# Performance work log

Measured on AMD Instinct MI355X. Metric: run time of the kernel, lower is better.

## Reference

```python
import jax, jax.numpy as jnp
import numpy as np

N_WIRES = 16
DIM = 2 ** N_WIRES
BSZ = 512
FFN_DIM = 64
N_BLOCKS = 2
N_RAND_OPS = 20
EPS = 1e-5


def rx_mat(theta):
    c = jnp.cos(theta / 2).astype(jnp.complex64)
    s = jnp.sin(theta / 2).astype(jnp.complex64)
    i = jnp.complex64(1j)
    return jnp.stack([jnp.stack([c, -i * s]), jnp.stack([-i * s, c])])


def ry_mat(theta):
    c = jnp.cos(theta / 2).astype(jnp.complex64)
    s = jnp.sin(theta / 2).astype(jnp.complex64)
    return jnp.stack([jnp.stack([c, -s]), jnp.stack([s, c])])


def apply_1q(psi, U, wire):
    # psi: [bsz, 2**n]; apply 2x2 U on `wire` (wire 0 = most significant)
    b = psi.shape[0]
    left = 2 ** wire
    s = psi.reshape(b, left, 2, -1)
    out = jnp.einsum('ij,bljr->blir', U, s)
    return out.reshape(b, -1)


def apply_cnot(psi, cw, tw):
    b = psi.shape[0]
    x = psi.reshape((b,) + (2,) * N_WIRES)
    x = jnp.moveaxis(x, (1 + cw, 1 + tw), (1, 2))
    x = jnp.concatenate([x[:, :1], x[:, 1:2, ::-1]], axis=1)
    x = jnp.moveaxis(x, (1, 2), (1 + cw, 1 + tw))
    return x.reshape(b, -1)


def measure_z(psi):
    # <Z_w> for every wire -> [bsz, n]
    b = psi.shape[0]
    p = jnp.abs(psi) ** 2
    outs = []
    for w in range(N_WIRES):
        pr = p.reshape(b, 2 ** w, 2, -1)
        outs.append((pr[:, :, 0] - pr[:, :, 1]).sum(axis=(1, 2)))
    return jnp.stack(outs, axis=1)


def layernorm(x, g, b):
    mu = x.mean(-1, keepdims=True)
    var = ((x - mu) ** 2).mean(-1, keepdims=True)
    return (x - mu) * jax.lax.rsqrt(var + EPS) * g + b


def setup_inputs() -> dict:
    key = jax.random.key(0)
    ks = jax.random.split(key, 16)
    states = jax.random.normal(ks[0], (BSZ, DIM), dtype=jnp.float32)
    rand_angles = jax.random.uniform(ks[1], (N_RAND_OPS,), minval=0.0, maxval=2 * np.pi, dtype=jnp.float32)
    theta_rx = jax.random.normal(ks[2], (N_BLOCKS,), dtype=jnp.float32)
    theta_ry = jax.random.normal(ks[3], (N_BLOCKS,), dtype=jnp.float32)
    s1 = 1.0 / np.sqrt(N_WIRES)
    s2 = 1.0 / np.sqrt(FFN_DIM)
    w1 = jax.random.uniform(ks[4], (N_BLOCKS, FFN_DIM, N_WIRES), minval=-s1, maxval=s1, dtype=jnp.float32)
    b1 = jax.random.uniform(ks[5], (N_BLOCKS, FFN_DIM), minval=-s1, maxval=s1, dtype=jnp.float32)
    w2 = jax.random.uniform(ks[6], (N_BLOCKS, N_WIRES, FFN_DIM), minval=-s2, maxval=s2, dtype=jnp.float32)
    b2 = jax.random.uniform(ks[7], (N_BLOCKS, N_WIRES), minval=-s2, maxval=s2, dtype=jnp.float32)
    g1 = jnp.ones((N_BLOCKS, N_WIRES), jnp.float32)
    be1 = jnp.zeros((N_BLOCKS, N_WIRES), jnp.float32)
    g2 = jnp.ones((N_BLOCKS, N_WIRES), jnp.float32)
    be2 = jnp.zeros((N_BLOCKS, N_WIRES), jnp.float32)
    wh = jax.random.uniform(ks[8], (1, N_WIRES), minval=-s1, maxval=s1, dtype=jnp.float32)
    bh = jax.random.uniform(ks[9], (1,), minval=-s1, maxval=s1, dtype=jnp.float32)
    return dict(states=states, rand_angles=rand_angles, theta_rx=theta_rx, theta_ry=theta_ry,
                w1=w1, b1=b1, w2=w2, b2=b2, g1=g1, be1=be1, g2=g2, be2=be2, wh=wh, bh=bh)


def _forward(states, rand_angles, theta_rx, theta_ry, w1, b1, w2, b2, g1, be1, g2, be2, wh, bh):
    # amplitude encoding: normalize, cast to complex statevector
    psi = (states / jnp.linalg.norm(states, axis=1, keepdims=True)).astype(jnp.complex64)
    # deterministic stand-in for tq.RandomLayer(n_ops=20): cycle RX/RY/CNOT over wires
    for i in range(N_RAND_OPS):
        w = (i * 5) % N_WIRES
        k = i % 3
        if k == 0:
            psi = apply_1q(psi, rx_mat(rand_angles[i]), w)
        elif k == 1:
            psi = apply_1q(psi, ry_mat(rand_angles[i]), w)
        else:
            psi = apply_cnot(psi, w, (w + 1) % N_WIRES)
    feats = None
    for blk in range(N_BLOCKS):
        # attention sub-module: shared RX on every wire, CNOT ring, measure Z
        Urx = rx_mat(theta_rx[blk])
        for w in range(N_WIRES):
            psi = apply_1q(psi, Urx, w)
        for w in range(N_WIRES - 1):
            psi = apply_cnot(psi, w, w + 1)
        psi = apply_cnot(psi, N_WIRES - 1, 0)
        attn = measure_z(psi)
        x = layernorm(attn, g1[blk], be1[blk])
        # ffn sub-module: shared RY on every wire, measure, MLP (dropout=eval identity)
        Ury = ry_mat(theta_ry[blk])
        for w in range(N_WIRES):
            psi = apply_1q(psi, Ury, w)
        m = measure_z(psi)
        h = jax.nn.relu(m @ w1[blk].T + b1[blk])
        ffn = h @ w2[blk].T + b2[blk]
        feats = layernorm(x + ffn, g2[blk], be2[blk])
    return (feats @ wh.T + bh)[:, 0]


def reference(states, rand_angles, theta_rx, theta_ry, w1, b1, w2, b2, g1, be1, g2, be2, wh, bh):
    return _forward(states, rand_angles, theta_rx, theta_ry, w1, b1, w2, b2, g1, be1, g2, be2, wh, bh)
```

## Files before the change

kernel.cpp:

```cpp
#include <hip/hip_runtime.h>
#include <math.h>


#define NT 256
#define ACCS 40
#define BSZQ 512

typedef float v2f __attribute__((ext_vector_type(2)));
typedef __fp16 h2t __attribute__((ext_vector_type(2)));

__device__ __forceinline__ v2f mk2(float a, float b){ v2f r; r.x = a; r.y = b; return r; }

__device__ __forceinline__ void wave_fence(){
  asm volatile("" ::: "memory");
  __builtin_amdgcn_wave_barrier();
  asm volatile("" ::: "memory");
}

__device__ __forceinline__ unsigned int f2h(v2f a){
  h2t h = __builtin_amdgcn_cvt_pkrtz(a.x, a.y);
  return *(unsigned int*)&h;
}
__device__ __forceinline__ v2f h2f(unsigned int u){
  h2t h = *(h2t*)&u;
  return mk2((float)h.x, (float)h.y);
}

__device__ __forceinline__ v2f pk_mul(v2f a, v2f b){
  v2f d; asm("v_pk_mul_f32 %0, %1, %2" : "=v"(d) : "v"(a), "v"(b)); return d;
}
__device__ __forceinline__ void pk_fma_acc(v2f& c, v2f a, v2f b){
  asm("v_pk_fma_f32 %0, %1, %2, %0" : "+v"(c) : "v"(a), "v"(b));
}
__device__ __forceinline__ void pk_fma_sw_acc(v2f& c, v2f a, v2f b){
  asm("v_pk_fma_f32 %0, %1, %2, %0 op_sel:[1,0,0] op_sel_hi:[0,1,1]"
      : "+v"(c) : "v"(a), "v"(b));
}
__device__ __forceinline__ void pk_add_acc(v2f& c, v2f a){
  asm("v_pk_add_f32 %0, %1, %0" : "+v"(c) : "v"(a));
}

struct C2 { float r, i; };
struct G1Q { C2 a, b, c, d; };

__device__ __forceinline__ C2 cmul(C2 x, C2 y){ return C2{ x.r*y.r - x.i*y.i, x.r*y.i + x.i*y.r }; }
__device__ __forceinline__ C2 cadd(C2 x, C2 y){ return C2{ x.r + y.r, x.i + y.i }; }
__device__ __forceinline__ G1Q mkRX(float th){
  float cc = cosf(0.5f*th), ss = sinf(0.5f*th);
  return G1Q{ C2{cc,0.f}, C2{0.f,-ss}, C2{0.f,-ss}, C2{cc,0.f} };
}
__device__ __forceinline__ G1Q mkRY(float th){
  float cc = cosf(0.5f*th), ss = sinf(0.5f*th);
  return G1Q{ C2{cc,0.f}, C2{-ss,0.f}, C2{ss,0.f}, C2{cc,0.f} };
}
__device__ __forceinline__ G1Q gmul(G1Q A, G1Q B){
  return G1Q{ cadd(cmul(A.a,B.a), cmul(A.b,B.c)),
              cadd(cmul(A.a,B.b), cmul(A.b,B.d)),
              cadd(cmul(A.c,B.a), cmul(A.d,B.c)),
              cadd(cmul(A.c,B.b), cmul(A.d,B.d)) };
}

struct PG1Q { v2f aR, aI, bR, bI, cR, cI, dR, dI; };
__device__ __forceinline__ PG1Q loadPG(const float* __restrict__ gt, int i){
  const float4* p = (const float4*)(gt + i*8);
  float4 u = p[0], w = p[1];
  PG1Q g;
  g.aR = mk2(u.x, u.x); g.aI = mk2(-u.y, u.y);
  g.bR = mk2(u.z, u.z); g.bI = mk2(-u.w, u.w);
  g.cR = mk2(w.x, w.x); g.cI = mk2(-w.y, w.y);
  g.dR = mk2(w.z, w.z); g.dI = mk2(-w.w, w.w);
  return g;
}

__device__ __forceinline__ int SW(int i){ return (i & ~15) | ((i ^ (i>>4) ^ (i>>8)) & 15); }

template<int M>
__device__ __forceinline__ float swzx(float x){
  return __int_as_float(__builtin_amdgcn_ds_swizzle(__float_as_int(x), (M<<10)|0x1F));
}
template<int C>
__device__ __forceinline__ float dppx(float x){
  return __int_as_float(__builtin_amdgcn_mov_dpp(__float_as_int(x), C, 0xF, 0xF, true));
}
template<int N>
__device__ __forceinline__ void wsumB(float* x){
  #pragma unroll
  for (int i=0;i<N;i++) x[i] += dppx<0xB1>(x[i]);
  #pragma unroll
  for (int i=0;i<N;i++) x[i] += dppx<0x4E>(x[i]);
  #pragma unroll
  for (int i=0;i<N;i++) x[i] += swzx<4>(x[i]);
  #pragma unroll
  for (int i=0;i<N;i++) x[i] += swzx<8>(x[i]);
  #pragma unroll
  for (int i=0;i<N;i++) x[i] += swzx<16>(x[i]);
  #pragma unroll
  for (int i=0;i<N;i++)
    x[i] = __int_as_float(__builtin_amdgcn_readlane(__float_as_int(x[i]), 0)) +
           __int_as_float(__builtin_amdgcn_readlane(__float_as_int(x[i]), 32));
}

__device__ __forceinline__ void greg16p(v2f* v, const PG1Q g, const int q){
  const int bq = 1<<q;
  #pragma unroll
  for (int r=0;r<16;r++){
    if (r & bq) continue;
    v2f a0 = v[r], a1 = v[r|bq];
    v2f t0 = pk_mul(a0, g.aR);
    pk_fma_sw_acc(t0, a0, g.aI);
    pk_fma_acc   (t0, a1, g.bR);
    pk_fma_sw_acc(t0, a1, g.bI);
    v2f t1 = pk_mul(a0, g.cR);
    pk_fma_sw_acc(t1, a0, g.cI);
    pk_fma_acc   (t1, a1, g.dR);
    pk_fma_sw_acc(t1, a1, g.dI);
    v[r] = t0; v[r|bq] = t1;
  }
}
__device__ __forceinline__ void creg16(v2f* v, const int qc, const int qt){
  #pragma unroll
  for (int r=0;r<16;r++){
    if ((r & (1<<qc)) && !(r & (1<<qt))){
      v2f tmp = v[r]; v[r] = v[r|(1<<qt)]; v[r|(1<<qt)] = tmp;
    }
  }
}
__device__ __forceinline__ float xdot16p(const v2f* v, const int m){
  v2f s = pk_mul(v[0], v[m]);
  #pragma unroll
  for (int r=1;r<16;r++) pk_fma_acc(s, v[r], v[r^m]);
  return s.x + s.y;
}

__global__ void qs_prep(const float* __restrict__ ra, const float* __restrict__ trx,
                        const float* __restrict__ tryv, float* __restrict__ gt){
  if (threadIdx.x != 0) return;
  float trx0 = trx[0];
  G1Q RX0 = mkRX(trx0);
  G1Q g[14];
  g[0]  = gmul(RX0, gmul(mkRY(ra[19]), mkRX(ra[3])));
  g[1]  = mkRX(trx0 + ra[6]);
  g[2]  = mkRX(trx0 + ra[9]);
  g[3]  = mkRX(trx0 + ra[12]);
  g[4]  = mkRX(trx0 + ra[15]);
  g[5]  = mkRX(trx0 + ra[18]);
  g[6]  = RX0;
  g[7]  = gmul(RX0, mkRY(ra[4]));
  g[8]  = mkRY(ra[1]);
  g[9]  = gmul(RX0, mkRY(ra[7]));
  g[10] = gmul(RX0, mkRY(ra[10]));
  g[11] = gmul(RX0, mkRY(ra[13]));
  g[12] = gmul(RX0, gmul(mkRY(ra[16]), mkRX(ra[0])));
  g[13] = gmul(mkRX(trx[1]), mkRY(tryv[0]));
  for (int i=0;i<14;i++){
    gt[i*8+0]=g[i].a.r; gt[i*8+1]=g[i].a.i;
    gt[i*8+2]=g[i].b.r; gt[i*8+3]=g[i].b.i;
    gt[i*8+4]=g[i].c.r; gt[i*8+5]=g[i].c.i;
    gt[i*8+6]=g[i].d.r; gt[i*8+7]=g[i].d.i;
  }
}

__global__ __launch_bounds__(NT) void qs_p1(const float* __restrict__ x, const float* __restrict__ gt,
                                            unsigned int* __restrict__ psi, float* __restrict__ acc){
  __shared__ __align__(16) v2f s[2048];
  int b = blockIdx.x >> 4, t = blockIdx.x & 15;
  int tid = threadIdx.x;
  if (t == 0 && tid < ACCS) acc[b*ACCS + tid] = 0.f;
  v2f v[16];
  const float4* xb = (const float4*)(x + (size_t)b*65536 + t*4096 + tid*16);
  #pragma unroll
  for (int q=0;q<4;q++){
    float4 f = xb[q];
    v[4*q+0] = mk2(f.x, 0.f);
    v[4*q+1] = mk2(f.y, 0.f);
    v[4*q+2] = mk2(f.z, 0.f);
    v[4*q+3] = mk2(f.w, 0.f);
  }
  greg16p(v, loadPG(gt,0), 0);
  greg16p(v, loadPG(gt,1), 1);
  greg16p(v, loadPG(gt,2), 2);
  greg16p(v, loadPG(gt,3), 3);
  {
    int wbase = ((tid&15)<<3) | ((tid>>4)<<7);
    int rbase = (tid&7) | ((tid>>4)<<7);
    v2f tmp[8];
    #pragma unroll
    for (int j=0;j<8;j++) s[SW(j | wbase)] = v[j];
    wave_fence();
    if (!(tid & 8)){
      #pragma unroll
      for (int r=0;r<8;r++)  v[r]     = s[SW(rbase | (r<<3))];
      #pragma unroll
      for (int r=8;r<16;r++) tmp[r-8] = s[SW(rbase | (r<<3))];
    }
    wave_fence();
    #pragma unroll
    for (int j=8;j<16;j++) s[SW((j&7) | wbase)] = v[j];
    wave_fence();
    if (tid & 8){
      #pragma unroll
      for (int r=0;r<16;r++) v[r] = s[SW(rbase | (r<<3))];
    } else {
      #pragma unroll
      for (int r=8;r<16;r++) v[r] = tmp[r-8];
    }
  }
  creg16(v, 1, 0);
  creg16(v, 2, 1);
  creg16(v, 3, 2);
  {
    bool c8 = (tid & 16);
    #pragma unroll
    for (int r=0;r<8;r++){
      v2f lo = v[r], hi = v[r|8];
      v[r]   = c8 ? hi : lo;
      v[r|8] = c8 ? lo : hi;
    }
  }
  greg16p(v, loadPG(gt,4), 0);
  greg16p(v, loadPG(gt,5), 1);
  PG1Q PG6 = loadPG(gt,6);
  greg16p(v, PG6, 2);
  greg16p(v, PG6, 3);
  unsigned int* pbL = psi + (size_t)b*65536 + t*4096;
  #pragma unroll
  for (int r=0;r<16;r++) pbL[(tid&15) | (r<<4) | ((tid>>4)<<8)] = f2h(v[r]);
}

__global__ __launch_bounds__(NT) void qs_p2(unsigned int* __restrict__ psi, const float* __restrict__ gt){
  __shared__ __align__(16) v2f s[2048];
  int b = blockIdx.x >> 4, t = blockIdx.x & 15;
  int tid = threadIdx.x;
  v2f v[16];
  unsigned int* pb = psi + (size_t)b*65536;
  #pragma unroll
  for (int r=0;r<16;r++)
    v[r] = h2f(pb[(tid&15) | (t<<4) | (r<<8) | ((tid>>4)<<12)]);
  greg16p(v, loadPG(gt,7), 3);
  greg16p(v, loadPG(gt,8), 2);
  creg16(v, 1, 0);
  creg16(v, 2, 1);
  PG1Q PG6 = loadPG(gt,6);
  greg16p(v, PG6, 2);
  greg16p(v, PG6, 1);
  greg16p(v, PG6, 0);
  {
    int wbase = ((tid>>4)&7) | ((tid&15)<<7);
    int rbase = ((tid>>4)<<3) | ((tid&15)<<7);
    v2f tmp[8];
    if (tid < 128){
      #pragma unroll
      for (int rr=0;rr<16;rr++) s[SW(wbase | (rr<<3))] = v[rr];
    }
    __syncthreads();
    #pragma unroll
    for (int r=0;r<8;r++) tmp[r] = s[SW(rbase | (r&7))];
    __syncthreads();
    if (tid >= 128){
      #pragma unroll
      for (int rr=0;rr<16;rr++) s[SW(wbase | (rr<<3))] = v[rr];
    }
    __syncthreads();
    #pragma unroll
    for (int r=8;r<16;r++) v[r] = s[SW(rbase | (r&7))];
    #pragma unroll
    for (int r=0;r<8;r++) v[r] = tmp[r];
  }
  greg16p(v, loadPG(gt,9), 0);
  greg16p(v, loadPG(gt,10), 1);
  greg16p(v, loadPG(gt,11), 2);
  greg16p(v, loadPG(gt,12), 3);
  #pragma unroll
  for (int r=0;r<16;r++)
    pb[(tid&15) | (t<<4) | ((tid>>4)<<8) | (r<<12)] = f2h(v[r]);
}

__global__ __launch_bounds__(NT) void qs_p4(unsigned int* __restrict__ psi, const float* __restrict__ gt,
                                            float* __restrict__ acc){
  __shared__ __align__(16) v2f s[2048];
  int b = blockIdx.x >> 4, t = blockIdx.x & 15;
  int tid = threadIdx.x;
  PG1Q U = loadPG(gt, 13);
  unsigned int* pb = psi + (size_t)b*65536;
  v2f v[16];
  {
    int Y = (tid>>4) | ((tid&15)<<4);
    int XH = Y ^ (Y>>1);
    int x7 = ((t>>3) ^ Y) & 1;
    int runbase = (XH<<8) | (x7<<7) | (((t ^ (t>>1)) & 7) << 4);
    const uint4* rp = (const uint4*)(pb + runbase);
    v2f tmp[16];
    #pragma unroll
    for (int q=0;q<4;q++){
      uint4 u = rp[q];
      tmp[4*q+0] = h2f(u.x);
      tmp[4*q+1] = h2f(u.y);
      tmp[4*q+2] = h2f(u.z);
      tmp[4*q+3] = h2f(u.w);
    }
    if (t & 1){
      v[15]=tmp[0];  v[14]=tmp[1];  v[12]=tmp[2];  v[13]=tmp[3];
      v[ 8]=tmp[4];  v[ 9]=tmp[5];  v[11]=tmp[6];  v[10]=tmp[7];
      v[ 0]=tmp[8];  v[ 1]=tmp[9];  v[ 3]=tmp[10]; v[ 2]=tmp[11];
      v[ 7]=tmp[12]; v[ 6]=tmp[13]; v[ 4]=tmp[14]; v[ 5]=tmp[15];
    } else {
      v[ 0]=tmp[0];  v[ 1]=tmp[1];  v[ 3]=tmp[2];  v[ 2]=tmp[3];
      v[ 7]=tmp[4];  v[ 6]=tmp[5];  v[ 4]=tmp[6];  v[ 5]=tmp[7];
      v[15]=tmp[8];  v[14]=tmp[9];  v[12]=tmp[10]; v[13]=tmp[11];
      v[ 8]=tmp[12]; v[ 9]=tmp[13]; v[11]=tmp[14]; v[10]=tmp[15];
    }
    #pragma unroll
    for (int r=1;r<16;r+=2){
      v[r].x = swzx<8>(v[r].x);
      v[r].y = swzx<8>(v[r].y);
    }
    greg16p(v, U, 0); greg16p(v, U, 1); greg16p(v, U, 2); greg16p(v, U, 3);
  }
  {
    int wbase = (tid&7) | ((tid>>4)<<7);
    int rbase = ((tid&15)<<3) | ((tid>>4)<<7);
    v2f tmp[8];
    if (!(tid & 8)){
      #pragma unroll
      for (int j=0;j<16;j++) s[SW(wbase | (j<<3))] = v[j];
    }
    wave_fence();
    #pragma unroll
    for (int r=0;r<8;r++) tmp[r] = s[SW((r&7) | rbase)];
    wave_fence();
    if (tid & 8){
      #pragma unroll
      for (int j=0;j<16;j++) s[SW(wbase | (j<<3))] = v[j];
    }
    wave_fence();
    #pragma unroll
    for (int r=8;r<16;r++) v[r] = s[SW((r&7) | rbase)];
    #pragma unroll
    for (int r=0;r<8;r++) v[r] = tmp[r];
  }
  float Xa, Xb, Xc, Xd;
  {
    greg16p(v, U, 0); greg16p(v, U, 1); greg16p(v, U, 2); greg16p(v, U, 3);
    creg16(v, 3, 2);
    creg16(v, 2, 1);
    creg16(v, 1, 0);
    Xa = xdot16p(v, 8);
    Xb = xdot16p(v, 4);
    Xc = xdot16p(v, 2);
    v2f XdP = mk2(0.f, 0.f);
    #pragma unroll
    for (int r=0;r<16;r++)
      pk_fma_acc(XdP, v[r], mk2(dppx<0xB1>(v[r^8].x), dppx<0xB1>(v[r^8].y)));
    Xd = XdP.x + XdP.y;
  }
  {
    int wbase = ((tid>>4)&7) | ((tid&15)<<7);
    int rbase = ((tid>>4)<<3) | ((tid&15)<<7);
    v2f tmp[8];
    __syncthreads();
    if (tid < 128){
      #pragma unroll
      for (int rr=0;rr<16;rr++) s[SW(wbase | (rr<<3))] = v[rr];
    }
    __syncthreads();
    #pragma unroll
    for (int r=0;r<8;r++) tmp[r] = s[SW(rbase | (r&7))];
    __syncthreads();
    if (tid >= 128){
      #pragma unroll
      for (int rr=0;rr<16;rr++) s[SW(wbase | (rr<<3))] = v[rr];
    }
    __syncthreads();
    #pragma unroll
    for (int r=8;r<16;r++) v[r] = s[SW(rbase | (r&7))];
    #pragma unroll
    for (int r=0;r<8;r++) v[r] = tmp[r];
  }
  float Xe, Xf, Xg, Xh;
  {
    greg16p(v, U, 0); greg16p(v, U, 1); greg16p(v, U, 2); greg16p(v, U, 3);
    {
      bool c12 = (tid & 16);
      #pragma unroll
      for (int r=0;r<8;r++){
        v2f lo = v[r], hi = v[r|8];
        v[r]   = c12 ? hi : lo;
        v[r|8] = c12 ? lo : hi;
      }
    }
    creg16(v, 3, 2);
    creg16(v, 2, 1);
    creg16(v, 1, 0);
    v2f XeP = mk2(0.f, 0.f);
    #pragma unroll
    for (int r=0;r<16;r++)
      pk_fma_acc(XeP, v[r], mk2(swzx<16>(v[r].x), swzx<16>(v[r].y)));
    Xe = XeP.x + XeP.y;
    Xf = xdot16p(v, 8);
    Xg = xdot16p(v, 4);
    Xh = xdot16p(v, 2);
    int Bs = (tid&15) | (t<<4) | ((tid>>4)<<12);
    int Cs = Bs ^ (Bs>>1);
    #pragma unroll
    for (int r=0;r<16;r++)
      pb[Cs ^ ((r<<8) ^ (r<<7))] = f2h(v[r]);
  }
  float vals[8] = {Xa, Xb, Xc, Xe, Xf, Xg, Xh, Xd};
  wsumB<8>(vals);
  if ((tid & 63) == 0){
    float* A = acc + b*ACCS;
    #pragma unroll
    for (int i=0;i<7;i++) atomicAdd(A+25+i, vals[i]);
    atomicAdd(A+32, vals[7]);
  }
}

__global__ __launch_bounds__(NT) void qs_p5(const unsigned int* __restrict__ psi, const float* __restrict__ gt,
                                            float* __restrict__ acc){
  int b = blockIdx.x >> 4, t = blockIdx.x & 15;
  int tid = threadIdx.x;
  PG1Q U = loadPG(gt, 13);
  const unsigned int* pb = psi + (size_t)b*65536;
  v2f v[16];
  int Bv = (t<<12) | ((tid>>4)<<8) | (tid&15);
  int Cg = Bv ^ (Bv>>1);
  #pragma unroll
  for (int r=0;r<16;r++)
    v[r] = h2f(pb[Cg ^ ((r<<4) ^ (r<<3))]);
  greg16p(v, U, 0); greg16p(v, U, 1); greg16p(v, U, 2); greg16p(v, U, 3);
  v2f z2 = mk2(0.f, 0.f);
  v2f totP=z2, S4P=z2, S5P=z2, S6P=z2, S7P=z2;
  #pragma unroll
  for (int r=0;r<16;r++){
    v2f sq = pk_mul(v[r], v[r]);
    pk_add_acc(totP, sq);
    if (__popc(r)&1)    pk_add_acc(S4P, sq);
    if (__popc(r>>1)&1) pk_add_acc(S5P, sq);
    if (__popc(r>>2)&1) pk_add_acc(S6P, sq);
    if (__popc(r>>3)&1) pk_add_acc(S7P, sq);
  }
  float totA = totP.x + totP.y;
  float S4l = S4P.x + S4P.y, S5l = S5P.x + S5P.y;
  float S6l = S6P.x + S6P.y, S7l = S7P.x + S7P.y;
  float S4h = totA - S4l;
  float S0 = (__popc(tid & 0x1F)&1) ? S4h : S4l;
  float S1 = (__popc(tid & 0x1E)&1) ? S4h : S4l;
  float S2 = (__popc(tid & 0x1C)&1) ? S4h : S4l;
  float S3 = (__popc(tid & 0x18)&1) ? S4h : S4l;
  bool u8 = (tid & 16);
  float S4 = u8 ? S4h : S4l;
  float S5 = u8 ? totA - S5l : S5l;
  float S6 = u8 ? totA - S6l : S6l;
  float S7 = u8 ? totA - S7l : S7l;
  float S8 = u8 ? totA : 0.f;
  float K9  = (tid & 32) ? totA : 0.f;
  float K10 = (tid & 64) ? totA : 0.f;
  float K11 = (tid & 128)? totA : 0.f;
  float X45 = xdot16p(v,3), X56 = xdot16p(v,6), X67 = xdot16p(v,12);
  v2f X01P=z2, X12P=z2, X23P=z2, X34P=z2, X78P=z2;
  #pragma unroll
  for (int r=0;r<16;r++){
    float vx = v[r].x, vy = v[r].y;
    pk_fma_acc(X01P, v[r], mk2(dppx<0x1B>(vx), dppx<0x1B>(vy)));
    pk_fma_acc(X12P, v[r], mk2(swzx<6>(vx),  swzx<6>(vy)));
    pk_fma_acc(X23P, v[r], mk2(swzx<12>(vx), swzx<12>(vy)));
    pk_fma_acc(X34P, v[r], mk2(swzx<8>(v[r^1].x), swzx<8>(v[r^1].y)));
    pk_fma_acc(X78P, v[r], mk2(swzx<16>(v[r^8].x), swzx<16>(v[r^8].y)));
  }
  float X01 = X01P.x + X01P.y, X12 = X12P.x + X12P.y, X23 = X23P.x + X23P.y;
  float X34 = X34P.x + X34P.y, X78 = X78P.x + X78P.y;
  float vals[21] = {totA, S0,S1,S2,S3,S4,S5,S6,S7,S8, K9,K10,K11,
                    X01,X12,X23,X34,X45,X56,X67,X78};
  wsumB<21>(vals);
  if ((tid & 63) == 0){
    float* A = acc + b*ACCS;
    atomicAdd(A+0, vals[0]);
    #pragma unroll
    for (int p=0;p<12;p++) atomicAdd(A+1+p, vals[1+p]);
    if (t&1) atomicAdd(A+13, vals[0]);
    if (t&2) atomicAdd(A+14, vals[0]);
    if (t&4) atomicAdd(A+15, vals[0]);
    float zz = vals[0] - 2.f*vals[1];
    if (t&8) zz = -zz;
    atomicAdd(A+16, zz);
    #pragma unroll
    for (int j=0;j<8;j++) atomicAdd(A+17+j, vals[13+j]);
  }
}

__global__ __launch_bounds__(256) void qs_tail(const float* __restrict__ acc, const float* __restrict__ tryv,
    const float* __restrict__ w1, const float* __restrict__ b1,
    const float* __restrict__ w2, const float* __restrict__ b2,
    const float* __restrict__ g1, const float* __restrict__ be1,
    const float* __restrict__ g2, const float* __restrict__ be2,
    const float* __restrict__ wh, const float* __restrict__ bh,
    float* __restrict__ out){
  int b = blockIdx.x * 256 + threadIdx.x;
  if (b >= BSZQ) return;
  const float* A = acc + b*ACCS;
  float tot = A[0];
  float inv = 1.f / tot;
  float Z[16], X[16];
  Z[0] = A[16] * inv;
  Z[1] = 1.f - 2.f*A[15]*inv;
  Z[2] = 1.f - 2.f*A[14]*inv;
  Z[3] = 1.f - 2.f*A[13]*inv;
  #pragma unroll
  for (int w=4; w<15; w++) Z[w] = 1.f - 2.f*A[1 + (15-w)]*inv;
  Z[15] = 1.f - 2.f*A[1]*inv;
  #pragma unroll
  for (int w=0; w<7; w++) X[w] = A[25+w]*inv;
  #pragma unroll
  for (int w=7; w<15; w++) X[w] = A[16 + (15-w)]*inv;
  X[15] = A[32]*inv;
  float th = tryv[1];
  float ct = cosf(th), st = sinf(th);
  float M4[16];
  #pragma unroll
  for (int w=0; w<16; w++) M4[w] = ct*Z[w] - st*X[w];
  float mu = 0.f;
  #pragma unroll
  for (int w=0; w<16; w++) mu += Z[w];
  mu *= (1.f/16.f);
  float var = 0.f;
  #pragma unroll
  for (int w=0; w<16; w++){ float d = Z[w]-mu; var += d*d; }
  var *= (1.f/16.f);
  float rs = rsqrtf(var + 1e-5f);
  float xln[16];
  #pragma unroll
  for (int w=0; w<16; w++) xln[w] = (Z[w]-mu)*rs*g1[16+w] + be1[16+w];
  float h[64];
  for (int j=0;j<64;j++){
    float sacc = b1[64 + j];
    #pragma unroll
    for (int w=0; w<16; w++) sacc += M4[w] * w1[1024 + j*16 + w];
    h[j] = fmaxf(sacc, 0.f);
  }
  float y[16];
  for (int w=0; w<16; w++){
    float sacc = b2[16 + w];
    #pragma unroll
    for (int j=0;j<64;j++) sacc += h[j] * w2[1024 + w*64 + j];
    y[w] = xln[w] + sacc;
  }
  mu = 0.f;
  #pragma unroll
  for (int w=0; w<16; w++) mu += y[w];
  mu *= (1.f/16.f);
  var = 0.f;
  #pragma unroll
  for (int w=0; w<16; w++){ float d = y[w]-mu; var += d*d; }
  var *= (1.f/16.f);
  rs = rsqrtf(var + 1e-5f);
  float o = bh[0];
  #pragma unroll
  for (int w=0; w<16; w++) o += ((y[w]-mu)*rs*g2[16+w] + be2[16+w]) * wh[w];
  out[b] = o;
}

extern "C" void kernel_launch(void* const* d_in, const int* in_sizes, int n_in,
                              void* d_out, int out_size, void* d_ws, size_t ws_size,
                              hipStream_t stream) {
  const float* states = (const float*)d_in[0];
  const float* ra     = (const float*)d_in[1];
  const float* trx    = (const float*)d_in[2];
  const float* tryv   = (const float*)d_in[3];
  const float* w1     = (const float*)d_in[4];
  const float* b1     = (const float*)d_in[5];
  const float* w2     = (const float*)d_in[6];
  const float* b2     = (const float*)d_in[7];
  const float* g1     = (const float*)d_in[8];
  const float* be1    = (const float*)d_in[9];
  const float* g2     = (const float*)d_in[10];
  const float* be2    = (const float*)d_in[11];
  const float* wh     = (const float*)d_in[12];
  const float* bh     = (const float*)d_in[13];
  float* out = (float*)d_out;

  unsigned int* psi = (unsigned int*)d_ws;
  float* acc  = (float*)((char*)d_ws + (size_t)BSZQ*65536*sizeof(float2));
  float* gt = out;

  dim3 g(BSZQ*16);
  qs_prep<<<1, 64, 0, stream>>>(ra, trx, tryv, gt);
  qs_p1<<<g, NT, 0, stream>>>(states, gt, psi, acc);
  qs_p2<<<g, NT, 0, stream>>>(psi, gt);
  qs_p4<<<g, NT, 0, stream>>>(psi, gt, acc);
  qs_p5<<<g, NT, 0, stream>>>(psi, gt, acc);
  qs_tail<<<2, 256, 0, stream>>>(acc, tryv, w1, b1, w2, b2, g1, be1, g2, be2, wh, bh, out);
}
```

Baseline: 535.8 us.

## Run gate math in packed fp16 and simplify LDS transposes in p2/p4/p5

Kernels p2, p4 and p5 now keep the state vector as packed half2 registers and apply gates with v_pk_fma_f16 instead of converting to fp32 and using v_pk_fma_f32. Expectation values use v_dot2_f32_f16, and the shared-memory transposes move 32-bit half2 words in a single pass with a new swizzle, rather than two staged passes of 64-bit values. Precomputed fp16 gate coefficients are stored after the fp32 table. This halves ALU work and LDS traffic and removes barriers, at the cost of fp16 rounding accumulating across gate applications.

After: 517.5 us. 3.4% less time.

```diff
diff --git a/kernel.cpp b/kernel.cpp
--- a/kernel.cpp
+++ b/kernel.cpp
@@ -17,13 +17,9 @@
   asm volatile("" ::: "memory");
 }
 
-__device__ __forceinline__ unsigned int f2h(v2f a){
+__device__ __forceinline__ unsigned f2h(v2f a){
   h2t h = __builtin_amdgcn_cvt_pkrtz(a.x, a.y);
-  return *(unsigned int*)&h;
-}
-__device__ __forceinline__ v2f h2f(unsigned int u){
-  h2t h = *(h2t*)&u;
-  return mk2((float)h.x, (float)h.y);
+  return *(unsigned*)&h;
 }
 
 __device__ __forceinline__ v2f pk_mul(v2f a, v2f b){
@@ -36,8 +32,19 @@
   asm("v_pk_fma_f32 %0, %1, %2, %0 op_sel:[1,0,0] op_sel_hi:[0,1,1]"
       : "+v"(c) : "v"(a), "v"(b));
 }
-__device__ __forceinline__ void pk_add_acc(v2f& c, v2f a){
-  asm("v_pk_add_f32 %0, %1, %0" : "+v"(c) : "v"(a));
+
+__device__ __forceinline__ unsigned pk16_mul(unsigned a, unsigned b){
+  unsigned d; asm("v_pk_mul_f16 %0, %1, %2" : "=v"(d) : "v"(a), "v"(b)); return d;
+}
+__device__ __forceinline__ void pk16_fma_acc(unsigned& c, unsigned a, unsigned b){
+  asm("v_pk_fma_f16 %0, %1, %2, %0" : "+v"(c) : "v"(a), "v"(b));
+}
+__device__ __forceinline__ void pk16_fma_sw_acc(unsigned& c, unsigned a, unsigned b){
+  asm("v_pk_fma_f16 %0, %1, %2, %0 op_sel:[1,0,0] op_sel_hi:[0,1,1]"
+      : "+v"(c) : "v"(a), "v"(b));
+}
+__device__ __forceinline__ void dot2acc(float& s, unsigned a, unsigned b){
+  asm("v_dot2_f32_f16 %0, %1, %2, %0" : "+v"(s) : "v"(a), "v"(b));
 }
 
 struct C2 { float r, i; };
@@ -71,12 +78,33 @@
   g.dR = mk2(w.z, w.z); g.dI = mk2(-w.w, w.w);
   return g;
 }
+struct PGH { unsigned aR, aI, bR, bI, cR, cI, dR, dI; };
+__device__ __forceinline__ PGH loadPGH(const float* __restrict__ gt, int i){
+  const uint4* p = (const uint4*)((const unsigned*)gt + 112 + i*8);
+  uint4 u = p[0], w = p[1];
+  return PGH{u.x, u.y, u.z, u.w, w.x, w.y, w.z, w.w};
+}
+__device__ __forceinline__ unsigned pkh(float lo, float hi){
+  __fp16 l = (__fp16)lo, h = (__fp16)hi;
+  unsigned short lb, hb;
+  __builtin_memcpy(&lb, &l, 2); __builtin_memcpy(&hb, &h, 2);
+  return (unsigned)lb | ((unsigned)hb<<16);
+}
 
 __device__ __forceinline__ int SW(int i){ return (i & ~15) | ((i ^ (i>>4) ^ (i>>8)) & 15); }
+__device__ __forceinline__ int SWB(int i){ return i ^ ((i>>8)&15) ^ (((i>>8)&1)<<4); }
 
 template<int M>
 __device__ __forceinline__ float swzx(float x){
   return __int_as_float(__builtin_amdgcn_ds_swizzle(__float_as_int(x), (M<<10)|0x1F));
+}
+template<int M>
+__device__ __forceinline__ unsigned swzu(unsigned x){
+  return (unsigned)__builtin_amdgcn_ds_swizzle((int)x, (M<<10)|0x1F);
+}
+template<int C>
+__device__ __forceinline__ unsigned dppu(unsigned x){
+  return (unsigned)__builtin_amdgcn_mov_dpp((int)x, C, 0xF, 0xF, true);
 }
 template<int C>
 __device__ __forceinline__ float dppx(float x){
@@ -117,6 +145,23 @@
     v[r] = t0; v[r|bq] = t1;
   }
 }
+__device__ __forceinline__ void greg16h(unsigned* v, const PGH g, const int q){
+  const int bq = 1<<q;
+  #pragma unroll
+  for (int r=0;r<16;r++){
+    if (r & bq) continue;
+    unsigned a0 = v[r], a1 = v[r|bq];
+    unsigned t0 = pk16_mul(a0, g.aR);
+    pk16_fma_sw_acc(t0, a0, g.aI);
+    pk16_fma_acc   (t0, a1, g.bR);
+    pk16_fma_sw_acc(t0, a1, g.bI);
+    unsigned t1 = pk16_mul(a0, g.cR);
+    pk16_fma_sw_acc(t1, a0, g.cI);
+    pk16_fma_acc   (t1, a1, g.dR);
+    pk16_fma_sw_acc(t1, a1, g.dI);
+    v[r] = t0; v[r|bq] = t1;
+  }
+}
 __device__ __forceinline__ void creg16(v2f* v, const int qc, const int qt){
   #pragma unroll
   for (int r=0;r<16;r++){
@@ -125,11 +170,19 @@
     }
   }
 }
-__device__ __forceinline__ float xdot16p(const v2f* v, const int m){
-  v2f s = pk_mul(v[0], v[m]);
-  #pragma unroll
-  for (int r=1;r<16;r++) pk_fma_acc(s, v[r], v[r^m]);
-  return s.x + s.y;
+__device__ __forceinline__ void creg16u(unsigned* v, const int qc, const int qt){
+  #pragma unroll
+  for (int r=0;r<16;r++){
+    if ((r & (1<<qc)) && !(r & (1<<qt))){
+      unsigned tmp = v[r]; v[r] = v[r|(1<<qt)]; v[r|(1<<qt)] = tmp;
+    }
+  }
+}
+__device__ __forceinline__ float xdot16h(const unsigned* v, const int m){
+  float s = 0.f;
+  #pragma unroll
+  for (int r=0;r<16;r++) dot2acc(s, v[r], v[r^m]);
+  return s;
 }
 
 __global__ void qs_prep(const float* __restrict__ ra, const float* __restrict__ trx,
@@ -158,10 +211,21 @@
     gt[i*8+4]=g[i].c.r; gt[i*8+5]=g[i].c.i;
     gt[i*8+6]=g[i].d.r; gt[i*8+7]=g[i].d.i;
   }
+  unsigned* gh = (unsigned*)gt + 112;
+  for (int i=0;i<14;i++){
+    gh[i*8+0] = pkh( g[i].a.r,  g[i].a.r);
+    gh[i*8+1] = pkh(-g[i].a.i,  g[i].a.i);
+    gh[i*8+2] = pkh( g[i].b.r,  g[i].b.r);
+    gh[i*8+3] = pkh(-g[i].b.i,  g[i].b.i);
+    gh[i*8+4] = pkh( g[i].c.r,  g[i].c.r);
+    gh[i*8+5] = pkh(-g[i].c.i,  g[i].c.i);
+    gh[i*8+6] = pkh( g[i].d.r,  g[i].d.r);
+    gh[i*8+7] = pkh(-g[i].d.i,  g[i].d.i);
+  }
 }
 
 __global__ __launch_bounds__(NT) void qs_p1(const float* __restrict__ x, const float* __restrict__ gt,
-                                            unsigned int* __restrict__ psi, float* __restrict__ acc){
+                                            unsigned* __restrict__ psi, float* __restrict__ acc){
   __shared__ __align__(16) v2f s[2048];
   int b = blockIdx.x >> 4, t = blockIdx.x & 15;
   int tid = threadIdx.x;
@@ -222,81 +286,65 @@
   PG1Q PG6 = loadPG(gt,6);
   greg16p(v, PG6, 2);
   greg16p(v, PG6, 3);
-  unsigned int* pbL = psi + (size_t)b*65536 + t*4096;
+  unsigned* pbL = psi + (size_t)b*65536 + t*4096;
   #pragma unroll
   for (int r=0;r<16;r++) pbL[(tid&15) | (r<<4) | ((tid>>4)<<8)] = f2h(v[r]);
 }
 
-__global__ __launch_bounds__(NT) void qs_p2(unsigned int* __restrict__ psi, const float* __restrict__ gt){
-  __shared__ __align__(16) v2f s[2048];
+__global__ __launch_bounds__(NT) void qs_p2(unsigned* __restrict__ psi, const float* __restrict__ gt){
+  __shared__ unsigned s[4096];
   int b = blockIdx.x >> 4, t = blockIdx.x & 15;
   int tid = threadIdx.x;
-  v2f v[16];
-  unsigned int* pb = psi + (size_t)b*65536;
+  int a = tid & 15, g = tid >> 4;
+  unsigned v[16];
+  unsigned* pb = psi + (size_t)b*65536;
   #pragma unroll
   for (int r=0;r<16;r++)
-    v[r] = h2f(pb[(tid&15) | (t<<4) | (r<<8) | ((tid>>4)<<12)]);
-  greg16p(v, loadPG(gt,7), 3);
-  greg16p(v, loadPG(gt,8), 2);
-  creg16(v, 1, 0);
-  creg16(v, 2, 1);
-  PG1Q PG6 = loadPG(gt,6);
-  greg16p(v, PG6, 2);
-  greg16p(v, PG6, 1);
-  greg16p(v, PG6, 0);
-  {
-    int wbase = ((tid>>4)&7) | ((tid&15)<<7);
-    int rbase = ((tid>>4)<<3) | ((tid&15)<<7);
-    v2f tmp[8];
-    if (tid < 128){
-      #pragma unroll
-      for (int rr=0;rr<16;rr++) s[SW(wbase | (rr<<3))] = v[rr];
-    }
-    __syncthreads();
-    #pragma unroll
-    for (int r=0;r<8;r++) tmp[r] = s[SW(rbase | (r&7))];
-    __syncthreads();
-    if (tid >= 128){
-      #pragma unroll
-      for (int rr=0;rr<16;rr++) s[SW(wbase | (rr<<3))] = v[rr];
-    }
-    __syncthreads();
-    #pragma unroll
-    for (int r=8;r<16;r++) v[r] = s[SW(rbase | (r&7))];
-    #pragma unroll
-    for (int r=0;r<8;r++) v[r] = tmp[r];
-  }
-  greg16p(v, loadPG(gt,9), 0);
-  greg16p(v, loadPG(gt,10), 1);
-  greg16p(v, loadPG(gt,11), 2);
-  greg16p(v, loadPG(gt,12), 3);
+    v[r] = pb[a | (t<<4) | (r<<8) | (g<<12)];
+  greg16h(v, loadPGH(gt,7), 3);
+  greg16h(v, loadPGH(gt,8), 2);
+  creg16u(v, 1, 0);
+  creg16u(v, 2, 1);
+  PGH G6 = loadPGH(gt,6);
+  greg16h(v, G6, 2);
+  greg16h(v, G6, 1);
+  greg16h(v, G6, 0);
+  #pragma unroll
+  for (int r=0;r<16;r++) s[SWB(a | (g<<4) | (r<<8))] = v[r];
+  __syncthreads();
+  #pragma unroll
+  for (int r=0;r<16;r++) v[r] = s[SWB(a | (r<<4) | (g<<8))];
+  greg16h(v, loadPGH(gt,9), 0);
+  greg16h(v, loadPGH(gt,10), 1);
+  greg16h(v, loadPGH(gt,11), 2);
+  greg16h(v, loadPGH(gt,12), 3);
   #pragma unroll
   for (int r=0;r<16;r++)
-    pb[(tid&15) | (t<<4) | ((tid>>4)<<8) | (r<<12)] = f2h(v[r]);
-}
-
-__global__ __launch_bounds__(NT) void qs_p4(unsigned int* __restrict__ psi, const float* __restrict__ gt,
+    pb[a | (t<<4) | (g<<8) | (r<<12)] = v[r];
+}
+
+__global__ __launch_bounds__(NT) void qs_p4(unsigned* __restrict__ psi, const float* __restrict__ gt,
                                             float* __restrict__ acc){
-  __shared__ __align__(16) v2f s[2048];
+  __shared__ unsigned s[4096];
   int b = blockIdx.x >> 4, t = blockIdx.x & 15;
   int tid = threadIdx.x;
-  PG1Q U = loadPG(gt, 13);
-  unsigned int* pb = psi + (size_t)b*65536;
-  v2f v[16];
+  PGH U = loadPGH(gt, 13);
+  unsigned* pb = psi + (size_t)b*65536;
+  unsigned v[16];
   {
     int Y = (tid>>4) | ((tid&15)<<4);
     int XH = Y ^ (Y>>1);
     int x7 = ((t>>3) ^ Y) & 1;
     int runbase = (XH<<8) | (x7<<7) | (((t ^ (t>>1)) & 7) << 4);
     const uint4* rp = (const uint4*)(pb + runbase);
-    v2f tmp[16];
+    unsigned tmp[16];
     #pragma unroll
     for (int q=0;q<4;q++){
       uint4 u = rp[q];
-      tmp[4*q+0] = h2f(u.x);
-      tmp[4*q+1] = h2f(u.y);
-      tmp[4*q+2] = h2f(u.z);
-      tmp[4*q+3] = h2f(u.w);
+      tmp[4*q+0] = u.x;
+      tmp[4*q+1] = u.y;
+      tmp[4*q+2] = u.z;
+      tmp[4*q+3] = u.w;
     }
     if (t & 1){
       v[15]=tmp[0];  v[14]=tmp[1];  v[12]=tmp[2];  v[13]=tmp[3];
@@ -310,100 +358,63 @@
       v[ 8]=tmp[12]; v[ 9]=tmp[13]; v[11]=tmp[14]; v[10]=tmp[15];
     }
     #pragma unroll
-    for (int r=1;r<16;r+=2){
-      v[r].x = swzx<8>(v[r].x);
-      v[r].y = swzx<8>(v[r].y);
-    }
-    greg16p(v, U, 0); greg16p(v, U, 1); greg16p(v, U, 2); greg16p(v, U, 3);
-  }
-  {
-    int wbase = (tid&7) | ((tid>>4)<<7);
-    int rbase = ((tid&15)<<3) | ((tid>>4)<<7);
-    v2f tmp[8];
-    if (!(tid & 8)){
-      #pragma unroll
-      for (int j=0;j<16;j++) s[SW(wbase | (j<<3))] = v[j];
-    }
-    wave_fence();
-    #pragma unroll
-    for (int r=0;r<8;r++) tmp[r] = s[SW((r&7) | rbase)];
-    wave_fence();
-    if (tid & 8){
-      #pragma unroll
-      for (int j=0;j<16;j++) s[SW(wbase | (j<<3))] = v[j];
-    }
-    wave_fence();
-    #pragma unroll
-    for (int r=8;r<16;r++) v[r] = s[SW((r&7) | rbase)];
-    #pragma unroll
-    for (int r=0;r<8;r++) v[r] = tmp[r];
-  }
+    for (int r=1;r<16;r+=2) v[r] = swzu<8>(v[r]);
+    greg16h(v, U, 0); greg16h(v, U, 1); greg16h(v, U, 2); greg16h(v, U, 3);
+    #pragma unroll
+    for (int j=0;j<16;j++)
+      s[SWB(j | ((tid>>4)<<4) | ((tid&15)<<8))] = v[j];
+  }
+  wave_fence();
   float Xa, Xb, Xc, Xd;
   {
-    greg16p(v, U, 0); greg16p(v, U, 1); greg16p(v, U, 2); greg16p(v, U, 3);
-    creg16(v, 3, 2);
-    creg16(v, 2, 1);
-    creg16(v, 1, 0);
-    Xa = xdot16p(v, 8);
-    Xb = xdot16p(v, 4);
-    Xc = xdot16p(v, 2);
-    v2f XdP = mk2(0.f, 0.f);
     #pragma unroll
     for (int r=0;r<16;r++)
-      pk_fma_acc(XdP, v[r], mk2(dppx<0xB1>(v[r^8].x), dppx<0xB1>(v[r^8].y)));
-    Xd = XdP.x + XdP.y;
-  }
-  {
-    int wbase = ((tid>>4)&7) | ((tid&15)<<7);
-    int rbase = ((tid>>4)<<3) | ((tid&15)<<7);
-    v2f tmp[8];
-    __syncthreads();
-    if (tid < 128){
-      #pragma unroll
-      for (int rr=0;rr<16;rr++) s[SW(wbase | (rr<<3))] = v[rr];
-    }
-    __syncthreads();
-    #pragma unroll
-    for (int r=0;r<8;r++) tmp[r] = s[SW(rbase | (r&7))];
-    __syncthreads();
-    if (tid >= 128){
-      #pragma unroll
-      for (int rr=0;rr<16;rr++) s[SW(wbase | (rr<<3))] = v[rr];
-    }
-    __syncthreads();
-    #pragma unroll
-    for (int r=8;r<16;r++) v[r] = s[SW(rbase | (r&7))];
-    #pragma unroll
-    for (int r=0;r<8;r++) v[r] = tmp[r];
-  }
+      v[r] = s[SWB((tid&15) | ((tid>>4)<<4) | (r<<8))];
+    greg16h(v, U, 0); greg16h(v, U, 1); greg16h(v, U, 2); greg16h(v, U, 3);
+    creg16u(v, 3, 2);
+    creg16u(v, 2, 1);
+    creg16u(v, 1, 0);
+    Xa = xdot16h(v, 8);
+    Xb = xdot16h(v, 4);
+    Xc = xdot16h(v, 2);
+    Xd = 0.f;
+    #pragma unroll
+    for (int r=0;r<16;r++) dot2acc(Xd, v[r], dppu<0xB1>(v[r^8]));
+    wave_fence();
+    #pragma unroll
+    for (int r=0;r<16;r++)
+      s[SWB((tid&15) | ((tid>>4)<<4) | (r<<8))] = v[r];
+  }
+  __syncthreads();
   float Xe, Xf, Xg, Xh;
   {
-    greg16p(v, U, 0); greg16p(v, U, 1); greg16p(v, U, 2); greg16p(v, U, 3);
+    #pragma unroll
+    for (int r=0;r<16;r++)
+      v[r] = s[SWB((tid&15) | (r<<4) | ((tid>>4)<<8))];
+    greg16h(v, U, 0); greg16h(v, U, 1); greg16h(v, U, 2); greg16h(v, U, 3);
     {
       bool c12 = (tid & 16);
       #pragma unroll
       for (int r=0;r<8;r++){
-        v2f lo = v[r], hi = v[r|8];
+        unsigned lo = v[r], hi = v[r|8];
         v[r]   = c12 ? hi : lo;
         v[r|8] = c12 ? lo : hi;
       }
     }
-    creg16(v, 3, 2);
-    creg16(v, 2, 1);
-    creg16(v, 1, 0);
-    v2f XeP = mk2(0.f, 0.f);
-    #pragma unroll
-    for (int r=0;r<16;r++)
-      pk_fma_acc(XeP, v[r], mk2(swzx<16>(v[r].x), swzx<16>(v[r].y)));
-    Xe = XeP.x + XeP.y;
-    Xf = xdot16p(v, 8);
-    Xg = xdot16p(v, 4);
-    Xh = xdot16p(v, 2);
+    creg16u(v, 3, 2);
+    creg16u(v, 2, 1);
+    creg16u(v, 1, 0);
+    Xe = 0.f;
+    #pragma unroll
+    for (int r=0;r<16;r++) dot2acc(Xe, v[r], swzu<16>(v[r]));
+    Xf = xdot16h(v, 8);
+    Xg = xdot16h(v, 4);
+    Xh = xdot16h(v, 2);
     int Bs = (tid&15) | (t<<4) | ((tid>>4)<<12);
     int Cs = Bs ^ (Bs>>1);
     #pragma unroll
     for (int r=0;r<16;r++)
-      pb[Cs ^ ((r<<8) ^ (r<<7))] = f2h(v[r]);
+      pb[Cs ^ ((r<<8) ^ (r<<7))] = v[r];
   }
   float vals[8] = {Xa, Xb, Xc, Xe, Xf, Xg, Xh, Xd};
   wsumB<8>(vals);
@@ -415,33 +426,28 @@
   }
 }
 
-__global__ __launch_bounds__(NT) void qs_p5(const unsigned int* __restrict__ psi, const float* __restrict__ gt,
+__global__ __launch_bounds__(NT) void qs_p5(const unsigned* __restrict__ psi, const float* __restrict__ gt,
                                             float* __restrict__ acc){
   int b = blockIdx.x >> 4, t = blockIdx.x & 15;
   int tid = threadIdx.x;
-  PG1Q U = loadPG(gt, 13);
-  const unsigned int* pb = psi + (size_t)b*65536;
-  v2f v[16];
+  PGH U = loadPGH(gt, 13);
+  const unsigned* pb = psi + (size_t)b*65536;
+  unsigned v[16];
   int Bv = (t<<12) | ((tid>>4)<<8) | (tid&15);
   int Cg = Bv ^ (Bv>>1);
   #pragma unroll
   for (int r=0;r<16;r++)
-    v[r] = h2f(pb[Cg ^ ((r<<4) ^ (r<<3))]);
-  greg16p(v, U, 0); greg16p(v, U, 1); greg16p(v, U, 2); greg16p(v, U, 3);
-  v2f z2 = mk2(0.f, 0.f);
-  v2f totP=z2, S4P=z2, S5P=z2, S6P=z2, S7P=z2;
+    v[r] = pb[Cg ^ ((r<<4) ^ (r<<3))];
+  greg16h(v, U, 0); greg16h(v, U, 1); greg16h(v, U, 2); greg16h(v, U, 3);
+  float totA=0.f, S4l=0.f, S5l=0.f, S6l=0.f, S7l=0.f;
   #pragma unroll
   for (int r=0;r<16;r++){
-    v2f sq = pk_mul(v[r], v[r]);
-    pk_add_acc(totP, sq);
-    if (__popc(r)&1)    pk_add_acc(S4P, sq);
-    if (__popc(r>>1)&1) pk_add_acc(S5P, sq);
-    if (__popc(r>>2)&1) pk_add_acc(S6P, sq);
-    if (__popc(r>>3)&1) pk_add_acc(S7P, sq);
-  }
-  float totA = totP.x + totP.y;
-  float S4l = S4P.x + S4P.y, S5l = S5P.x + S5P.y;
-  float S6l = S6P.x + S6P.y, S7l = S7P.x + S7P.y;
+    dot2acc(totA, v[r], v[r]);
+    if (__popc(r)&1)    dot2acc(S4l, v[r], v[r]);
+    if (__popc(r>>1)&1) dot2acc(S5l, v[r], v[r]);
+    if (__popc(r>>2)&1) dot2acc(S6l, v[r], v[r]);
+    if (__popc(r>>3)&1) dot2acc(S7l, v[r], v[r]);
+  }
   float S4h = totA - S4l;
   float S0 = (__popc(tid & 0x1F)&1) ? S4h : S4l;
   float S1 = (__popc(tid & 0x1E)&1) ? S4h : S4l;
@@ -456,19 +462,16 @@
   float K9  = (tid & 32) ? totA : 0.f;
   float K10 = (tid & 64) ? totA : 0.f;
   float K11 = (tid & 128)? totA : 0.f;
-  float X45 = xdot16p(v,3), X56 = xdot16p(v,6), X67 = xdot16p(v,12);
-  v2f X01P=z2, X12P=z2, X23P=z2, X34P=z2, X78P=z2;
+  float X45 = xdot16h(v,3), X56 = xdot16h(v,6), X67 = xdot16h(v,12);
+  float X01=0.f, X12=0.f, X23=0.f, X34=0.f, X78=0.f;
   #pragma unroll
   for (int r=0;r<16;r++){
-    float vx = v[r].x, vy = v[r].y;
-    pk_fma_acc(X01P, v[r], mk2(dppx<0x1B>(vx), dppx<0x1B>(vy)));
-    pk_fma_acc(X12P, v[r], mk2(swzx<6>(vx),  swzx<6>(vy)));
-    pk_fma_acc(X23P, v[r], mk2(swzx<12>(vx), swzx<12>(vy)));
-    pk_fma_acc(X34P, v[r], mk2(swzx<8>(v[r^1].x), swzx<8>(v[r^1].y)));
-    pk_fma_acc(X78P, v[r], mk2(swzx<16>(v[r^8].x), swzx<16>(v[r^8].y)));
-  }
-  float X01 = X01P.x + X01P.y, X12 = X12P.x + X12P.y, X23 = X23P.x + X23P.y;
-  float X34 = X34P.x + X34P.y, X78 = X78P.x + X78P.y;
+    dot2acc(X01, v[r], dppu<0x1B>(v[r]));
+    dot2acc(X12, v[r], swzu<6>(v[r]));
+    dot2acc(X23, v[r], swzu<12>(v[r]));
+    dot2acc(X34, v[r], swzu<8>(v[r^1]));
+    dot2acc(X78, v[r], swzu<16>(v[r^8]));
+  }
   float vals[21] = {totA, S0,S1,S2,S3,S4,S5,S6,S7,S8, K9,K10,K11,
                     X01,X12,X23,X34,X45,X56,X67,X78};
   wsumB<21>(vals);
@@ -578,7 +581,7 @@
   const float* bh     = (const float*)d_in[13];
   float* out = (float*)d_out;
 
-  unsigned int* psi = (unsigned int*)d_ws;
+  unsigned* psi = (unsigned*)d_ws;
   float* acc  = (float*)((char*)d_ws + (size_t)BSZQ*65536*sizeof(float2));
   float* gt = out;
 
```
